# Optimization experiments

Hardware: AMD Instinct MI355X
Metric: run time of the kernel (lower is better)

## Reference

```python
import jax, jax.numpy as jnp
import numpy as np

NEG_INF = -1e30  # stand-in for float('-inf') that is safe under softmax


def setup_inputs() -> dict:
    key = jax.random.key(0)
    k1, k2, k3, k4 = jax.random.split(key, 4)
    B, T, C, H = 4, 4096, 1024, 128
    x = jax.random.normal(k1, (B, T, C), dtype=jnp.float32)
    # nn.Linear(n_emb, head_size, bias=False): store as [C, H] so y = x @ W
    Wk = jax.random.normal(k2, (C, H), dtype=jnp.float32) * (C ** -0.5)
    Wq = jax.random.normal(k3, (C, H), dtype=jnp.float32) * (C ** -0.5)
    Wv = jax.random.normal(k4, (C, H), dtype=jnp.float32) * (C ** -0.5)
    return {"x": x, "Wk": Wk, "Wq": Wq, "Wv": Wv}


def reference(x, Wk, Wq, Wv):
    B, T, C = x.shape
    k = x @ Wk  # [B, T, H]
    q = x @ Wq  # [B, T, H]
    v = x @ Wv  # [B, T, H]
    # Faithful to original: wei = k @ q^T, scaled by C**-0.5 (C = n_emb)
    wei = jnp.einsum('bih,bjh->bij', k, q) * (C ** -0.5)  # [B, T, T]
    causal = jnp.tril(jnp.ones((T, T), dtype=bool))
    wei = jnp.where(causal, wei, NEG_INF)
    wei = jax.nn.softmax(wei, axis=-1)
    out = jnp.einsum('bij,bjh->bih', wei, v)  # [B, T, H]
    return out
```

## Files before the change

### kernel.cpp

```cpp
#include <hip/hip_runtime.h>
#include <hip/hip_bf16.h>

#define T_SEQ 4096
#define NBATCH 4
#define C_EMB 1024
#define H_DIM 128
#define M_ROWS (NBATCH * T_SEQ)
#define SPLIT 4

typedef __bf16 bf16x8 __attribute__((ext_vector_type(8)));
typedef float  floatx4 __attribute__((ext_vector_type(4)));

__device__ __forceinline__ ushort f2bf(float f) {
    __hip_bfloat16 h = __float2bfloat16(f);
    return *reinterpret_cast<ushort*>(&h);
}
__device__ __forceinline__ float bf2f(ushort u) {
    unsigned int v = ((unsigned int)u) << 16;
    return *reinterpret_cast<float*>(&v);
}
__device__ __forceinline__ uint4 pack8(const float4& a, const float4& b) {
    __hip_bfloat162 h0 = __float22bfloat162_rn(make_float2(a.x, a.y));
    __hip_bfloat162 h1 = __float22bfloat162_rn(make_float2(a.z, a.w));
    __hip_bfloat162 h2 = __float22bfloat162_rn(make_float2(b.x, b.y));
    __hip_bfloat162 h3 = __float22bfloat162_rn(make_float2(b.z, b.w));
    uint4 r;
    r.x = *reinterpret_cast<unsigned int*>(&h0);
    r.y = *reinterpret_cast<unsigned int*>(&h1);
    r.z = *reinterpret_cast<unsigned int*>(&h2);
    r.w = *reinterpret_cast<unsigned int*>(&h3);
    return r;
}
__device__ __forceinline__ void gld16(const ushort* g, ushort* l) {
    __builtin_amdgcn_global_load_lds(
        (const __attribute__((address_space(1))) unsigned int*)(g),
        (__attribute__((address_space(3))) unsigned int*)(l),
        16, 0, 0);
}

__global__ __launch_bounds__(256) void transpose_w(
    const float* __restrict__ Wk, const float* __restrict__ Wq,
    const float* __restrict__ Wv, ushort* __restrict__ wt) {
    const int z = blockIdx.y;
    const float* W = (z == 0) ? Wk : (z == 1) ? Wq : Wv;
    ushort* Wtz = wt + (size_t)z * H_DIM * C_EMB;
    int linear = blockIdx.x * 256 + threadIdx.x;
    int n  = linear >> 7;
    int k0 = (linear & 127) << 3;
    ushort tmp[8];
#pragma unroll
    for (int j = 0; j < 8; ++j)
        tmp[j] = f2bf(W[(size_t)(k0 + j) * H_DIM + n]);
    uint4 pk;
    pk.x = (unsigned int)tmp[0] | ((unsigned int)tmp[1] << 16);
    pk.y = (unsigned int)tmp[2] | ((unsigned int)tmp[3] << 16);
    pk.z = (unsigned int)tmp[4] | ((unsigned int)tmp[5] << 16);
    pk.w = (unsigned int)tmp[6] | ((unsigned int)tmp[7] << 16);
    *reinterpret_cast<uint4*>(Wtz + (size_t)n * C_EMB + k0) = pk;
}

__global__ __launch_bounds__(256, 3) void qkv_gemm(
    const float* __restrict__ x, const ushort* __restrict__ wt,
    ushort* __restrict__ kqv) {
    const int z  = blockIdx.y;
    const int m0 = blockIdx.x * 64;
    const ushort* Wtz = wt + (size_t)z * H_DIM * C_EMB;

    __shared__ ushort As[64 * 64];
    __shared__ ushort Bs[128 * 64];

    const int tid  = threadIdx.x;
    const int lane = tid & 63;
    const int wave = tid >> 6;
    const int l15  = lane & 15;
    const int quad = lane >> 4;

    floatx4 acc[8];
#pragma unroll
    for (int ni = 0; ni < 8; ++ni) acc[ni] = floatx4{0.f, 0.f, 0.f, 0.f};

    for (int kt = 0; kt < 16; ++kt) {
        __syncthreads();
#pragma unroll
        for (int i = 0; i < 4; ++i) {
            int row = wave * 32 + i * 8 + (lane >> 3);
            int chg = (lane & 7) ^ (row & 7);
            gld16(Wtz + (size_t)row * C_EMB + kt * 64 + chg * 8,
                  Bs + (wave * 32 + i * 8) * 64);
        }
#pragma unroll
        for (int i = 0; i < 2; ++i) {
            int u = i * 256 + tid;
            int r = u >> 3, ch = u & 7;
            const float* src = x + (size_t)(m0 + r) * C_EMB + kt * 64 + ch * 8;
            float4 v0 = *reinterpret_cast<const float4*>(src);
            float4 v1 = *reinterpret_cast<const float4*>(src + 4);
            int chp = ch ^ (r & 7);
            *reinterpret_cast<uint4*>(As + r * 64 + chp * 8) = pack8(v0, v1);
        }
        __syncthreads();

#pragma unroll
        for (int kk = 0; kk < 2; ++kk) {
            bf16x8 a = *reinterpret_cast<const bf16x8*>(
                As + (wave * 16 + l15) * 64 + ((4 * kk + quad) ^ (l15 & 7)) * 8);
#pragma unroll
            for (int ni = 0; ni < 8; ++ni) {
                bf16x8 b = *reinterpret_cast<const bf16x8*>(
                    Bs + (ni * 16 + l15) * 64 + ((4 * kk + quad) ^ (l15 & 7)) * 8);
                acc[ni] = __builtin_amdgcn_mfma_f32_16x16x32_bf16(a, b, acc[ni], 0, 0, 0);
            }
        }
    }

    if (z < 2) {
        const float scale = (z == 0) ? 0.03125f : 1.0f;
        ushort* outz = kqv + (size_t)z * M_ROWS * H_DIM;
#pragma unroll
        for (int ni = 0; ni < 8; ++ni)
#pragma unroll
            for (int r = 0; r < 4; ++r) {
                int row = m0 + wave * 16 + quad * 4 + r;
                int col = ni * 16 + l15;
                outz[(size_t)row * H_DIM + col] = f2bf(acc[ni][r] * scale);
            }
    } else {
        ushort* vt = kqv + (size_t)2 * M_ROWS * H_DIM;
        int trow = m0 + wave * 16 + quad * 4;
        int bb   = trow >> 12;
        int tloc = trow & (T_SEQ - 1);
#pragma unroll
        for (int ni = 0; ni < 8; ++ni) {
            int h = ni * 16 + l15;
            ushort4 pk;
            pk.x = f2bf(acc[ni][0]);
            pk.y = f2bf(acc[ni][1]);
            pk.z = f2bf(acc[ni][2]);
            pk.w = f2bf(acc[ni][3]);
            *reinterpret_cast<ushort4*>(
                vt + ((size_t)(bb * H_DIM + h) << 12) + tloc) = pk;
        }
    }
}

#define P_STRIDE 72
__global__ __launch_bounds__(256, 3) void flash_chunk(
    const ushort* __restrict__ kqv, ushort* __restrict__ partO,
    float* __restrict__ partML) {
    const int it = blockIdx.x >> 2;
    const int c  = blockIdx.x & 3;
    if (c > it) return;
    const int b  = blockIdx.y;
    const int i0 = it * 64;

    const ushort* Qg = kqv + (size_t)b * T_SEQ * H_DIM;
    const ushort* Kg = kqv + (size_t)M_ROWS * H_DIM + (size_t)b * T_SEQ * H_DIM;
    const ushort* Vt = kqv + (size_t)2 * M_ROWS * H_DIM + (size_t)b * H_DIM * T_SEQ;

    __shared__ ushort Ks[64 * 128];
    __shared__ ushort Vs[128 * 64];
    __shared__ ushort Ps[4][16 * P_STRIDE];

    const int tid  = threadIdx.x;
    const int lane = tid & 63;
    const int wave = tid >> 6;
    const int l15  = lane & 15;
    const int quad = lane >> 4;

    bf16x8 q[4];
    {
        const ushort* qrow = Qg + (size_t)(i0 + wave * 16 + l15) * H_DIM + quad * 8;
#pragma unroll
        for (int kk = 0; kk < 4; ++kk)
            q[kk] = *reinterpret_cast<const bf16x8*>(qrow + kk * 32);
    }

    float m_i[4], l_i[4];
#pragma unroll
    for (int r = 0; r < 4; ++r) { m_i[r] = -1e30f; l_i[r] = 0.f; }
    floatx4 o[8];
#pragma unroll
    for (int nh = 0; nh < 8; ++nh) o[nh] = floatx4{0.f, 0.f, 0.f, 0.f};

    ushort* Pw = Ps[wave];

    for (int jt = c; jt <= it; jt += SPLIT) {
        const int j0 = jt * 64;
        __syncthreads();
#pragma unroll
        for (int i = 0; i < 4; ++i) {
            int row = wave * 16 + i * 4 + (lane >> 4);
            int chg = (lane & 15) ^ (row & 15);
            gld16(Kg + (size_t)(j0 + row) * H_DIM + chg * 8,
                  Ks + (wave * 16 + i * 4) * 128);
        }
#pragma unroll
        for (int i = 0; i < 4; ++i) {
            int row = wave * 32 + i * 8 + (lane >> 3);
            int chg = (lane & 7) ^ (row & 7);
            gld16(Vt + (size_t)row * T_SEQ + j0 + chg * 8,
                  Vs + (wave * 32 + i * 8) * 64);
        }
        __syncthreads();

        floatx4 s[4];
#pragma unroll
        for (int ni = 0; ni < 4; ++ni) s[ni] = floatx4{0.f, 0.f, 0.f, 0.f};
#pragma unroll
        for (int kk = 0; kk < 4; ++kk)
#pragma unroll
            for (int ni = 0; ni < 4; ++ni) {
                bf16x8 kb = *reinterpret_cast<const bf16x8*>(
                    Ks + (ni * 16 + l15) * 128 + ((4 * kk + quad) ^ l15) * 8);
                s[ni] = __builtin_amdgcn_mfma_f32_16x16x32_bf16(q[kk], kb, s[ni], 0, 0, 0);
            }

        if (jt == it) {
            int ii = i0 + wave * 16 + quad * 4;
#pragma unroll
            for (int ni = 0; ni < 4; ++ni) {
                int j = j0 + ni * 16 + l15;
#pragma unroll
                for (int r = 0; r < 4; ++r)
                    if (j > ii + r) s[ni][r] = -1e30f;
            }
        }

        float alpha[4], rs[4];
#pragma unroll
        for (int r = 0; r < 4; ++r) {
            float v = fmaxf(fmaxf(s[0][r], s[1][r]), fmaxf(s[2][r], s[3][r]));
#pragma unroll
            for (int off = 8; off >= 1; off >>= 1)
                v = fmaxf(v, __shfl_xor(v, off, 64));
            float mn = fmaxf(m_i[r], v);
            alpha[r] = __expf(m_i[r] - mn);
            m_i[r] = mn;
            rs[r] = 0.f;
        }
#pragma unroll
        for (int ni = 0; ni < 4; ++ni)
#pragma unroll
            for (int r = 0; r < 4; ++r) {
                float p = __expf(s[ni][r] - m_i[r]);
                rs[r] += p;
                Pw[(quad * 4 + r) * P_STRIDE + ni * 16 + l15] = f2bf(p);
            }
#pragma unroll
        for (int r = 0; r < 4; ++r) {
            float v = rs[r];
#pragma unroll
            for (int off = 8; off >= 1; off >>= 1)
                v += __shfl_xor(v, off, 64);
            l_i[r] = l_i[r] * alpha[r] + v;
        }
#pragma unroll
        for (int nh = 0; nh < 8; ++nh)
#pragma unroll
            for (int r = 0; r < 4; ++r) o[nh][r] *= alpha[r];

#pragma unroll
        for (int kp = 0; kp < 2; ++kp) {
            bf16x8 a = *reinterpret_cast<const bf16x8*>(
                Pw + l15 * P_STRIDE + kp * 32 + quad * 8);
#pragma unroll
            for (int nh = 0; nh < 8; ++nh) {
                bf16x8 vb = *reinterpret_cast<const bf16x8*>(
                    Vs + (nh * 16 + l15) * 64 + ((4 * kp + quad) ^ (l15 & 7)) * 8);
                o[nh] = __builtin_amdgcn_mfma_f32_16x16x32_bf16(a, vb, o[nh], 0, 0, 0);
            }
        }
    }

    const int idx = ((b * 64 + it) << 2) + c;
    ushort* po = partO + (size_t)idx * 64 * 128;
#pragma unroll
    for (int nh = 0; nh < 8; ++nh)
#pragma unroll
        for (int r = 0; r < 4; ++r) {
            int row = wave * 16 + quad * 4 + r;
            po[(size_t)row * 128 + nh * 16 + l15] = f2bf(o[nh][r]);
        }
    if (l15 == 0) {
        float* ml = partML + (size_t)idx * 128;
#pragma unroll
        for (int r = 0; r < 4; ++r) {
            int row = wave * 16 + quad * 4 + r;
            ml[row]      = m_i[r];
            ml[64 + row] = l_i[r];
        }
    }
}

__global__ __launch_bounds__(256) void combine(
    const ushort* __restrict__ partO, const float* __restrict__ partML,
    float* __restrict__ out) {
    const int it = blockIdx.x, b = blockIdx.y;
    const int count = min(SPLIT, it + 1);
    const int tid = threadIdx.x;
    const int row = tid >> 2;
    const int cg  = (tid & 3) * 32;
    const int base = (b * 64 + it) << 2;

    float m_c[SPLIT], l_c[SPLIT];
    float M = -1e30f;
    for (int cc = 0; cc < count; ++cc) {
        const float* ml = partML + (size_t)(base + cc) * 128;
        m_c[cc] = ml[row];
        l_c[cc] = ml[64 + row];
        M = fmaxf(M, m_c[cc]);
    }
    float L = 0.f, w[SPLIT];
    for (int cc = 0; cc < count; ++cc) {
        w[cc] = __expf(m_c[cc] - M);
        L += w[cc] * l_c[cc];
    }

    float acc[32];
#pragma unroll
    for (int j = 0; j < 32; ++j) acc[j] = 0.f;
    for (int cc = 0; cc < count; ++cc) {
        const ushort* po = partO + (size_t)(base + cc) * 8192 + (size_t)row * 128 + cg;
        float wc = w[cc];
#pragma unroll
        for (int g = 0; g < 4; ++g) {
            uint4 v = *reinterpret_cast<const uint4*>(po + g * 8);
            const ushort* pv = reinterpret_cast<const ushort*>(&v);
#pragma unroll
            for (int e = 0; e < 8; ++e)
                acc[g * 8 + e] += wc * bf2f(pv[e]);
        }
    }
    float invL = 1.0f / L;
    float* op = out + ((size_t)b * T_SEQ + it * 64 + row) * H_DIM + cg;
#pragma unroll
    for (int g = 0; g < 8; ++g) {
        float4 v;
        v.x = acc[g * 4 + 0] * invL;
        v.y = acc[g * 4 + 1] * invL;
        v.z = acc[g * 4 + 2] * invL;
        v.w = acc[g * 4 + 3] * invL;
        *reinterpret_cast<float4*>(op + g * 4) = v;
    }
}

extern "C" void kernel_launch(void* const* d_in, const int* in_sizes, int n_in,
                              void* d_out, int out_size, void* d_ws, size_t ws_size,
                              hipStream_t stream) {
    const float* x  = (const float*)d_in[0];
    const float* Wk = (const float*)d_in[1];
    const float* Wq = (const float*)d_in[2];
    const float* Wv = (const float*)d_in[3];

    ushort* kqv    = (ushort*)d_ws;
    ushort* wt     = kqv + (size_t)3 * M_ROWS * H_DIM;
    ushort* partO  = wt + (size_t)3 * H_DIM * C_EMB;
    float*  partML = (float*)(partO + (size_t)1024 * 64 * 128);

    transpose_w<<<dim3(64, 3), 256, 0, stream>>>(Wk, Wq, Wv, wt);
    qkv_gemm<<<dim3(256, 3), 256, 0, stream>>>(x, wt, kqv);
    flash_chunk<<<dim3(64 * SPLIT, NBATCH), 256, 0, stream>>>(kqv, partO, partML);
    combine<<<dim3(64, NBATCH), 256, 0, stream>>>(partO, partML, (float*)d_out);
}
```

Measured before the change: 183.2 us.

## Fuse QKV GEMM across heads and double flash query tile to 128 rows

The QKV projection now computes all three weight matrices in one block per 64-row tile, so x is read and converted once instead of three times. The flash kernel processes 128 query rows per block (two 16-row MFMA tiles per wave), which reuses each K/V tile across twice as many queries, and it schedules the heaviest causal tiles first. The combine kernel is rewritten to match the new partial layout, with normalisation weights precomputed in shared memory. The cost is more registers and LDS, which is why occupancy hints drop to 2, and there are fewer blocks to spread across CUs.

```diff
diff --git a/kernel.cpp b/kernel.cpp
--- a/kernel.cpp
+++ b/kernel.cpp
@@ -59,15 +59,13 @@
     *reinterpret_cast<uint4*>(Wtz + (size_t)n * C_EMB + k0) = pk;
 }
 
-__global__ __launch_bounds__(256, 3) void qkv_gemm(
+__global__ __launch_bounds__(256, 2) void qkv_gemm(
     const float* __restrict__ x, const ushort* __restrict__ wt,
     ushort* __restrict__ kqv) {
-    const int z  = blockIdx.y;
     const int m0 = blockIdx.x * 64;
-    const ushort* Wtz = wt + (size_t)z * H_DIM * C_EMB;
 
     __shared__ ushort As[64 * 64];
-    __shared__ ushort Bs[128 * 64];
+    __shared__ ushort Bs[384 * 64];
 
     const int tid  = threadIdx.x;
     const int lane = tid & 63;
@@ -75,18 +73,21 @@
     const int l15  = lane & 15;
     const int quad = lane >> 4;
 
-    floatx4 acc[8];
-#pragma unroll
-    for (int ni = 0; ni < 8; ++ni) acc[ni] = floatx4{0.f, 0.f, 0.f, 0.f};
+    floatx4 acc[4][6];
+#pragma unroll
+    for (int mi = 0; mi < 4; ++mi)
+#pragma unroll
+        for (int ni = 0; ni < 6; ++ni)
+            acc[mi][ni] = floatx4{0.f, 0.f, 0.f, 0.f};
 
     for (int kt = 0; kt < 16; ++kt) {
         __syncthreads();
 #pragma unroll
-        for (int i = 0; i < 4; ++i) {
-            int row = wave * 32 + i * 8 + (lane >> 3);
+        for (int i = 0; i < 12; ++i) {
+            int row = wave * 96 + i * 8 + (lane >> 3);
             int chg = (lane & 7) ^ (row & 7);
-            gld16(Wtz + (size_t)row * C_EMB + kt * 64 + chg * 8,
-                  Bs + (wave * 32 + i * 8) * 64);
+            gld16(wt + (size_t)row * C_EMB + kt * 64 + chg * 8,
+                  Bs + (wave * 96 + i * 8) * 64);
         }
 #pragma unroll
         for (int i = 0; i < 2; ++i) {
@@ -95,63 +96,72 @@
             const float* src = x + (size_t)(m0 + r) * C_EMB + kt * 64 + ch * 8;
             float4 v0 = *reinterpret_cast<const float4*>(src);
             float4 v1 = *reinterpret_cast<const float4*>(src + 4);
-            int chp = ch ^ (r & 7);
-            *reinterpret_cast<uint4*>(As + r * 64 + chp * 8) = pack8(v0, v1);
+            *reinterpret_cast<uint4*>(As + r * 64 + (ch ^ (r & 7)) * 8) = pack8(v0, v1);
         }
         __syncthreads();
 
 #pragma unroll
         for (int kk = 0; kk < 2; ++kk) {
-            bf16x8 a = *reinterpret_cast<const bf16x8*>(
-                As + (wave * 16 + l15) * 64 + ((4 * kk + quad) ^ (l15 & 7)) * 8);
-#pragma unroll
-            for (int ni = 0; ni < 8; ++ni) {
+            bf16x8 a[4];
+#pragma unroll
+            for (int mi = 0; mi < 4; ++mi)
+                a[mi] = *reinterpret_cast<const bf16x8*>(
+                    As + (mi * 16 + l15) * 64 + ((4 * kk + quad) ^ (l15 & 7)) * 8);
+#pragma unroll
+            for (int ni = 0; ni < 6; ++ni) {
                 bf16x8 b = *reinterpret_cast<const bf16x8*>(
-                    Bs + (ni * 16 + l15) * 64 + ((4 * kk + quad) ^ (l15 & 7)) * 8);
-                acc[ni] = __builtin_amdgcn_mfma_f32_16x16x32_bf16(a, b, acc[ni], 0, 0, 0);
-            }
-        }
-    }
-
-    if (z < 2) {
-        const float scale = (z == 0) ? 0.03125f : 1.0f;
-        ushort* outz = kqv + (size_t)z * M_ROWS * H_DIM;
-#pragma unroll
-        for (int ni = 0; ni < 8; ++ni)
-#pragma unroll
-            for (int r = 0; r < 4; ++r) {
-                int row = m0 + wave * 16 + quad * 4 + r;
-                int col = ni * 16 + l15;
-                outz[(size_t)row * H_DIM + col] = f2bf(acc[ni][r] * scale);
-            }
-    } else {
-        ushort* vt = kqv + (size_t)2 * M_ROWS * H_DIM;
-        int trow = m0 + wave * 16 + quad * 4;
-        int bb   = trow >> 12;
-        int tloc = trow & (T_SEQ - 1);
-#pragma unroll
-        for (int ni = 0; ni < 8; ++ni) {
-            int h = ni * 16 + l15;
-            ushort4 pk;
-            pk.x = f2bf(acc[ni][0]);
-            pk.y = f2bf(acc[ni][1]);
-            pk.z = f2bf(acc[ni][2]);
-            pk.w = f2bf(acc[ni][3]);
-            *reinterpret_cast<ushort4*>(
-                vt + ((size_t)(bb * H_DIM + h) << 12) + tloc) = pk;
+                    Bs + (wave * 96 + ni * 16 + l15) * 64 + ((4 * kk + quad) ^ (l15 & 7)) * 8);
+#pragma unroll
+                for (int mi = 0; mi < 4; ++mi)
+                    acc[mi][ni] = __builtin_amdgcn_mfma_f32_16x16x32_bf16(a[mi], b, acc[mi][ni], 0, 0, 0);
+            }
+        }
+    }
+
+    ushort* vt = kqv + (size_t)2 * M_ROWS * H_DIM;
+#pragma unroll
+    for (int ni = 0; ni < 6; ++ni) {
+        const int ng = wave * 96 + ni * 16;
+        const int z  = ng >> 7;
+        const int nz = (ng & 127) + l15;
+        if (z < 2) {
+            const float scale = (z == 0) ? 0.03125f : 1.0f;
+            ushort* outz = kqv + (size_t)z * M_ROWS * H_DIM;
+#pragma unroll
+            for (int mi = 0; mi < 4; ++mi)
+#pragma unroll
+                for (int r = 0; r < 4; ++r) {
+                    int row = m0 + mi * 16 + quad * 4 + r;
+                    outz[(size_t)row * H_DIM + nz] = f2bf(acc[mi][ni][r] * scale);
+                }
+        } else {
+#pragma unroll
+            for (int mi = 0; mi < 4; ++mi) {
+                int trow = m0 + mi * 16 + quad * 4;
+                int bb   = trow >> 12;
+                int tloc = trow & (T_SEQ - 1);
+                ushort4 pk;
+                pk.x = f2bf(acc[mi][ni][0]);
+                pk.y = f2bf(acc[mi][ni][1]);
+                pk.z = f2bf(acc[mi][ni][2]);
+                pk.w = f2bf(acc[mi][ni][3]);
+                *reinterpret_cast<ushort4*>(
+                    vt + ((size_t)(bb * H_DIM + nz) << 12) + tloc) = pk;
+            }
         }
     }
 }
 
 #define P_STRIDE 72
-__global__ __launch_bounds__(256, 3) void flash_chunk(
+__global__ __launch_bounds__(256, 2) void flash_chunk(
     const ushort* __restrict__ kqv, ushort* __restrict__ partO,
     float* __restrict__ partML) {
-    const int it = blockIdx.x >> 2;
+    const int it = 31 - (blockIdx.x >> 2);
     const int c  = blockIdx.x & 3;
-    if (c > it) return;
+    const int jtmax = 2 * it + 1;
+    if (c > jtmax) return;
     const int b  = blockIdx.y;
-    const int i0 = it * 64;
+    const int i0 = it * 128;
 
     const ushort* Qg = kqv + (size_t)b * T_SEQ * H_DIM;
     const ushort* Kg = kqv + (size_t)M_ROWS * H_DIM + (size_t)b * T_SEQ * H_DIM;
@@ -159,7 +169,7 @@
 
     __shared__ ushort Ks[64 * 128];
     __shared__ ushort Vs[128 * 64];
-    __shared__ ushort Ps[4][16 * P_STRIDE];
+    __shared__ ushort Ps[4][32 * P_STRIDE];
 
     const int tid  = threadIdx.x;
     const int lane = tid & 63;
@@ -167,24 +177,29 @@
     const int l15  = lane & 15;
     const int quad = lane >> 4;
 
-    bf16x8 q[4];
-    {
-        const ushort* qrow = Qg + (size_t)(i0 + wave * 16 + l15) * H_DIM + quad * 8;
+    bf16x8 q[2][4];
+#pragma unroll
+    for (int mi = 0; mi < 2; ++mi) {
+        const ushort* qrow = Qg + (size_t)(i0 + wave * 32 + mi * 16 + l15) * H_DIM + quad * 8;
 #pragma unroll
         for (int kk = 0; kk < 4; ++kk)
-            q[kk] = *reinterpret_cast<const bf16x8*>(qrow + kk * 32);
-    }
-
-    float m_i[4], l_i[4];
-#pragma unroll
-    for (int r = 0; r < 4; ++r) { m_i[r] = -1e30f; l_i[r] = 0.f; }
-    floatx4 o[8];
-#pragma unroll
-    for (int nh = 0; nh < 8; ++nh) o[nh] = floatx4{0.f, 0.f, 0.f, 0.f};
+            q[mi][kk] = *reinterpret_cast<const bf16x8*>(qrow + kk * 32);
+    }
+
+    float m_i[2][4], l_i[2][4];
+#pragma unroll
+    for (int mi = 0; mi < 2; ++mi)
+#pragma unroll
+        for (int r = 0; r < 4; ++r) { m_i[mi][r] = -1e30f; l_i[mi][r] = 0.f; }
+    floatx4 o[2][8];
+#pragma unroll
+    for (int mi = 0; mi < 2; ++mi)
+#pragma unroll
+        for (int nh = 0; nh < 8; ++nh) o[mi][nh] = floatx4{0.f, 0.f, 0.f, 0.f};
 
     ushort* Pw = Ps[wave];
 
-    for (int jt = c; jt <= it; jt += SPLIT) {
+    for (int jt = c; jt <= jtmax; jt += SPLIT) {
         const int j0 = jt * 64;
         __syncthreads();
 #pragma unroll
@@ -203,92 +218,114 @@
         }
         __syncthreads();
 
-        floatx4 s[4];
-#pragma unroll
-        for (int ni = 0; ni < 4; ++ni) s[ni] = floatx4{0.f, 0.f, 0.f, 0.f};
+        floatx4 s[2][4];
+#pragma unroll
+        for (int mi = 0; mi < 2; ++mi)
+#pragma unroll
+            for (int ni = 0; ni < 4; ++ni) s[mi][ni] = floatx4{0.f, 0.f, 0.f, 0.f};
 #pragma unroll
         for (int kk = 0; kk < 4; ++kk)
 #pragma unroll
             for (int ni = 0; ni < 4; ++ni) {
                 bf16x8 kb = *reinterpret_cast<const bf16x8*>(
                     Ks + (ni * 16 + l15) * 128 + ((4 * kk + quad) ^ l15) * 8);
-                s[ni] = __builtin_amdgcn_mfma_f32_16x16x32_bf16(q[kk], kb, s[ni], 0, 0, 0);
-            }
-
-        if (jt == it) {
-            int ii = i0 + wave * 16 + quad * 4;
-#pragma unroll
-            for (int ni = 0; ni < 4; ++ni) {
-                int j = j0 + ni * 16 + l15;
-#pragma unroll
-                for (int r = 0; r < 4; ++r)
-                    if (j > ii + r) s[ni][r] = -1e30f;
-            }
-        }
-
-        float alpha[4], rs[4];
-#pragma unroll
-        for (int r = 0; r < 4; ++r) {
-            float v = fmaxf(fmaxf(s[0][r], s[1][r]), fmaxf(s[2][r], s[3][r]));
-#pragma unroll
-            for (int off = 8; off >= 1; off >>= 1)
-                v = fmaxf(v, __shfl_xor(v, off, 64));
-            float mn = fmaxf(m_i[r], v);
-            alpha[r] = __expf(m_i[r] - mn);
-            m_i[r] = mn;
-            rs[r] = 0.f;
-        }
-#pragma unroll
-        for (int ni = 0; ni < 4; ++ni)
+                s[0][ni] = __builtin_amdgcn_mfma_f32_16x16x32_bf16(q[0][kk], kb, s[0][ni], 0, 0, 0);
+                s[1][ni] = __builtin_amdgcn_mfma_f32_16x16x32_bf16(q[1][kk], kb, s[1][ni], 0, 0, 0);
+            }
+
+        if (jt >= 2 * it) {
+#pragma unroll
+            for (int mi = 0; mi < 2; ++mi) {
+                int rbase = i0 + wave * 32 + mi * 16 + quad * 4;
+#pragma unroll
+                for (int ni = 0; ni < 4; ++ni) {
+                    int j = j0 + ni * 16 + l15;
+#pragma unroll
+                    for (int r = 0; r < 4; ++r)
+                        if (j > rbase + r) s[mi][ni][r] = -1e30f;
+                }
+            }
+        }
+
+        float alpha[2][4], rs[2][4];
+#pragma unroll
+        for (int mi = 0; mi < 2; ++mi)
 #pragma unroll
             for (int r = 0; r < 4; ++r) {
-                float p = __expf(s[ni][r] - m_i[r]);
-                rs[r] += p;
-                Pw[(quad * 4 + r) * P_STRIDE + ni * 16 + l15] = f2bf(p);
-            }
-#pragma unroll
-        for (int r = 0; r < 4; ++r) {
-            float v = rs[r];
-#pragma unroll
-            for (int off = 8; off >= 1; off >>= 1)
-                v += __shfl_xor(v, off, 64);
-            l_i[r] = l_i[r] * alpha[r] + v;
-        }
-#pragma unroll
-        for (int nh = 0; nh < 8; ++nh)
-#pragma unroll
-            for (int r = 0; r < 4; ++r) o[nh][r] *= alpha[r];
+                float v = fmaxf(fmaxf(s[mi][0][r], s[mi][1][r]),
+                                fmaxf(s[mi][2][r], s[mi][3][r]));
+#pragma unroll
+                for (int off = 8; off >= 1; off >>= 1)
+                    v = fmaxf(v, __shfl_xor(v, off, 64));
+                float mn = fmaxf(m_i[mi][r], v);
+                alpha[mi][r] = __expf(m_i[mi][r] - mn);
+                m_i[mi][r] = mn;
+                rs[mi][r] = 0.f;
+            }
+#pragma unroll
+        for (int mi = 0; mi < 2; ++mi)
+#pragma unroll
+            for (int ni = 0; ni < 4; ++ni)
+#pragma unroll
+                for (int r = 0; r < 4; ++r) {
+                    float p = __expf(s[mi][ni][r] - m_i[mi][r]);
+                    rs[mi][r] += p;
+                    Pw[(mi * 16 + quad * 4 + r) * P_STRIDE + ni * 16 + l15] = f2bf(p);
+                }
+#pragma unroll
+        for (int mi = 0; mi < 2; ++mi)
+#pragma unroll
+            for (int r = 0; r < 4; ++r) {
+                float v = rs[mi][r];
+#pragma unroll
+                for (int off = 8; off >= 1; off >>= 1)
+                    v += __shfl_xor(v, off, 64);
+                l_i[mi][r] = l_i[mi][r] * alpha[mi][r] + v;
+            }
+#pragma unroll
+        for (int mi = 0; mi < 2; ++mi)
+#pragma unroll
+            for (int nh = 0; nh < 8; ++nh)
+#pragma unroll
+                for (int r = 0; r < 4; ++r) o[mi][nh][r] *= alpha[mi][r];
 
 #pragma unroll
         for (int kp = 0; kp < 2; ++kp) {
-            bf16x8 a = *reinterpret_cast<const bf16x8*>(
-                Pw + l15 * P_STRIDE + kp * 32 + quad * 8);
+            bf16x8 a0 = *reinterpret_cast<const bf16x8*>(
+                Pw + (l15) * P_STRIDE + kp * 32 + quad * 8);
+            bf16x8 a1 = *reinterpret_cast<const bf16x8*>(
+                Pw + (16 + l15) * P_STRIDE + kp * 32 + quad * 8);
 #pragma unroll
             for (int nh = 0; nh < 8; ++nh) {
                 bf16x8 vb = *reinterpret_cast<const bf16x8*>(
                     Vs + (nh * 16 + l15) * 64 + ((4 * kp + quad) ^ (l15 & 7)) * 8);
-                o[nh] = __builtin_amdgcn_mfma_f32_16x16x32_bf16(a, vb, o[nh], 0, 0, 0);
-            }
-        }
-    }
-
-    const int idx = ((b * 64 + it) << 2) + c;
-    ushort* po = partO + (size_t)idx * 64 * 128;
-#pragma unroll
-    for (int nh = 0; nh < 8; ++nh)
-#pragma unroll
-        for (int r = 0; r < 4; ++r) {
-            int row = wave * 16 + quad * 4 + r;
-            po[(size_t)row * 128 + nh * 16 + l15] = f2bf(o[nh][r]);
-        }
+                o[0][nh] = __builtin_amdgcn_mfma_f32_16x16x32_bf16(a0, vb, o[0][nh], 0, 0, 0);
+                o[1][nh] = __builtin_amdgcn_mfma_f32_16x16x32_bf16(a1, vb, o[1][nh], 0, 0, 0);
+            }
+        }
+    }
+
+    const int idx = ((b * 32 + it) << 2) + c;
+    ushort* po = partO + (size_t)idx * 128 * 128;
+#pragma unroll
+    for (int mi = 0; mi < 2; ++mi)
+#pragma unroll
+        for (int nh = 0; nh < 8; ++nh)
+#pragma unroll
+            for (int r = 0; r < 4; ++r) {
+                int row = wave * 32 + mi * 16 + quad * 4 + r;
+                po[(size_t)row * 128 + nh * 16 + l15] = f2bf(o[mi][nh][r]);
+            }
     if (l15 == 0) {
-        float* ml = partML + (size_t)idx * 128;
-#pragma unroll
-        for (int r = 0; r < 4; ++r) {
-            int row = wave * 16 + quad * 4 + r;
-            ml[row]      = m_i[r];
-            ml[64 + row] = l_i[r];
-        }
+        float* ml = partML + (size_t)idx * 256;
+#pragma unroll
+        for (int mi = 0; mi < 2; ++mi)
+#pragma unroll
+            for (int r = 0; r < 4; ++r) {
+                int row = wave * 32 + mi * 16 + quad * 4 + r;
+                ml[row]       = m_i[mi][r];
+                ml[128 + row] = l_i[mi][r];
+            }
     }
 }
 
@@ -296,51 +333,48 @@
     const ushort* __restrict__ partO, const float* __restrict__ partML,
     float* __restrict__ out) {
     const int it = blockIdx.x, b = blockIdx.y;
-    const int count = min(SPLIT, it + 1);
+    const int count = min(SPLIT, 2 * it + 2);
     const int tid = threadIdx.x;
-    const int row = tid >> 2;
-    const int cg  = (tid & 3) * 32;
-    const int base = (b * 64 + it) << 2;
-
-    float m_c[SPLIT], l_c[SPLIT];
-    float M = -1e30f;
-    for (int cc = 0; cc < count; ++cc) {
-        const float* ml = partML + (size_t)(base + cc) * 128;
-        m_c[cc] = ml[row];
-        l_c[cc] = ml[64 + row];
-        M = fmaxf(M, m_c[cc]);
-    }
-    float L = 0.f, w[SPLIT];
-    for (int cc = 0; cc < count; ++cc) {
-        w[cc] = __expf(m_c[cc] - M);
-        L += w[cc] * l_c[cc];
-    }
-
-    float acc[32];
-#pragma unroll
-    for (int j = 0; j < 32; ++j) acc[j] = 0.f;
-    for (int cc = 0; cc < count; ++cc) {
-        const ushort* po = partO + (size_t)(base + cc) * 8192 + (size_t)row * 128 + cg;
-        float wc = w[cc];
-#pragma unroll
-        for (int g = 0; g < 4; ++g) {
-            uint4 v = *reinterpret_cast<const uint4*>(po + g * 8);
-            const ushort* pv = reinterpret_cast<const ushort*>(&v);
-#pragma unroll
-            for (int e = 0; e < 8; ++e)
-                acc[g * 8 + e] += wc * bf2f(pv[e]);
-        }
-    }
-    float invL = 1.0f / L;
-    float* op = out + ((size_t)b * T_SEQ + it * 64 + row) * H_DIM + cg;
-#pragma unroll
-    for (int g = 0; g < 8; ++g) {
-        float4 v;
-        v.x = acc[g * 4 + 0] * invL;
-        v.y = acc[g * 4 + 1] * invL;
-        v.z = acc[g * 4 + 2] * invL;
-        v.w = acc[g * 4 + 3] * invL;
-        *reinterpret_cast<float4*>(op + g * 4) = v;
+    const int base = (b * 32 + it) << 2;
+
+    __shared__ float wS[SPLIT][128];
+    if (tid < 128) {
+        const int row = tid;
+        float mv[SPLIT], lv[SPLIT];
+        float M = -1e30f;
+        for (int cc = 0; cc < count; ++cc) {
+            mv[cc] = partML[(size_t)(base + cc) * 256 + row];
+            lv[cc] = partML[(size_t)(base + cc) * 256 + 128 + row];
+            M = fmaxf(M, mv[cc]);
+        }
+        float L = 0.f;
+        for (int cc = 0; cc < count; ++cc) {
+            float e = __expf(mv[cc] - M);
+            wS[cc][row] = e;
+            L += e * lv[cc];
+        }
+        float invL = 1.0f / L;
+        for (int cc = 0; cc < count; ++cc) wS[cc][row] *= invL;
+    }
+    __syncthreads();
+
+    float* outb = out + ((size_t)b * T_SEQ + it * 128) * H_DIM;
+#pragma unroll
+    for (int rep = 0; rep < 16; ++rep) {
+        int idx = rep * 256 + tid;
+        int row = idx >> 5;
+        int cg  = (idx & 31) * 4;
+        float4 acc = make_float4(0.f, 0.f, 0.f, 0.f);
+        for (int cc = 0; cc < count; ++cc) {
+            ushort4 p = *reinterpret_cast<const ushort4*>(
+                partO + (size_t)(base + cc) * 16384 + (size_t)row * 128 + cg);
+            float w = wS[cc][row];
+            acc.x += w * bf2f(p.x);
+            acc.y += w * bf2f(p.y);
+            acc.z += w * bf2f(p.z);
+            acc.w += w * bf2f(p.w);
+        }
+        *reinterpret_cast<float4*>(outb + (size_t)row * H_DIM + cg) = acc;
     }
 }
 
@@ -355,10 +389,10 @@
     ushort* kqv    = (ushort*)d_ws;
     ushort* wt     = kqv + (size_t)3 * M_ROWS * H_DIM;
     ushort* partO  = wt + (size_t)3 * H_DIM * C_EMB;
-    float*  partML = (float*)(partO + (size_t)1024 * 64 * 128);
+    float*  partML = (float*)(partO + (size_t)512 * 128 * 128);
 
     transpose_w<<<dim3(64, 3), 256, 0, stream>>>(Wk, Wq, Wv, wt);
-    qkv_gemm<<<dim3(256, 3), 256, 0, stream>>>(x, wt, kqv);
-    flash_chunk<<<dim3(64 * SPLIT, NBATCH), 256, 0, stream>>>(kqv, partO, partML);
-    combine<<<dim3(64, NBATCH), 256, 0, stream>>>(partO, partML, (float*)d_out);
-}
+    qkv_gemm<<<dim3(256), 256, 0, stream>>>(x, wt, kqv);
+    flash_chunk<<<dim3(32 * SPLIT, NBATCH), 256, 0, stream>>>(kqv, partO, partML);
+    combine<<<dim3(32, NBATCH), 256, 0, stream>>>(partO, partML, (float*)d_out);
+}
```

Result: slower. 210.0 us (+14.6%).
